# Optimization experiments

Hardware: AMD Instinct MI355X
Metric: run time of the kernel (lower is better)

Reference implementation:

```python
import jax, jax.numpy as jnp
import numpy as np

N_NODES = 100000
N_EDGES = 3200000
DIM = 64


def setup_inputs() -> dict:
    key = jax.random.key(0)
    k1, k2, k3, k4, k5, k6 = jax.random.split(key, 6)
    lap_rows = jax.random.randint(k1, (N_EDGES,), 0, N_NODES, dtype=jnp.int32)
    lap_cols = jax.random.randint(k2, (N_EDGES,), 0, N_NODES, dtype=jnp.int32)
    # normalized-Laplacian-like positive values
    lap_vals = jax.random.uniform(k3, (N_EDGES,), dtype=jnp.float32) * 0.1
    features = jax.random.normal(k4, (N_NODES, DIM), dtype=jnp.float32)
    scale = 1.0 / np.sqrt(DIM)
    W1 = jax.random.normal(k5, (DIM, DIM), dtype=jnp.float32) * scale
    b1 = jnp.zeros((DIM,), dtype=jnp.float32)
    W2 = jax.random.normal(k6, (DIM, DIM), dtype=jnp.float32) * scale
    b2 = jnp.zeros((DIM,), dtype=jnp.float32)
    return {
        "lap_rows": lap_rows, "lap_cols": lap_cols, "lap_vals": lap_vals,
        "features": features, "W1": W1, "b1": b1, "W2": W2, "b2": b2,
    }


def reference(lap_rows, lap_cols, lap_vals, features, W1, b1, W2, b2):
    # x = L @ features  (COO SpMM: gather source rows, scale, scatter-add to dest)
    msgs = lap_vals[:, None] * features[lap_cols]            # [E, D]
    x = jax.ops.segment_sum(msgs, lap_rows, num_segments=N_NODES)  # [N, D]
    # output = (L+I) E W1 + (L E * E) W2
    inter_part1 = (features + x) @ W1 + b1                   # [N, D_out]
    inter_part2 = (x * features) @ W2 + b2                   # [N, D_out]
    return inter_part1 + inter_part2
```

## Files before the change

kernel.cpp:

```cpp
#include <hip/hip_runtime.h>
#include <hip/hip_fp16.h>

#define DIM 64
#define RPB 64
#define RPB_SHIFT 6
#define SUP_SHIFT 11
#define SB_MAX 64
#define CAP 3072
#define CAPK (CAP / 1024)
#define HTILE_H 16384
#define HTILE1 8192
#define HTILE2 4096

typedef _Float16 half8 __attribute__((ext_vector_type(8)));
typedef float    f32x4 __attribute__((ext_vector_type(4)));
typedef float    f32x2 __attribute__((ext_vector_type(2)));

template <bool HI>
__device__ __forceinline__ __half2 q2h(unsigned int w)
{
    f32x2 f = __builtin_amdgcn_cvt_pk_f32_fp8(w, HI);
    return __floats2half2_rn(f[0], f[1]);
}

__global__ __launch_bounds__(256) void scatter_kernel(
    const int* __restrict__ rows, const int* __restrict__ cols,
    const float* __restrict__ vals, const float* __restrict__ feat,
    float* __restrict__ x, int E)
{
    unsigned long long t = (unsigned long long)blockIdx.x * blockDim.x + threadIdx.x;
    int e = (int)(t >> 6);
    int d = (int)(t & 63);
    if (e >= E) return;
    int r = rows[e];
    int c = cols[e];
    float v = vals[e];
    float f = feat[(size_t)c * DIM + d];
    atomicAdd(&x[(size_t)r * DIM + d], v * f);
}

__global__ __launch_bounds__(256) void cvt_kernel(
    const float* __restrict__ f, __half* __restrict__ h, int n2)
{
    int i = blockIdx.x * blockDim.x + threadIdx.x;
    if (i < n2) {
        float2 v = ((const float2*)f)[i];
        __half2 o;
        o.x = __float2half(v.x);
        o.y = __float2half(v.y);
        ((__half2*)h)[i] = o;
    }
}

__global__ __launch_bounds__(1024) void prep_kernel(
    const float* __restrict__ feat, __half* __restrict__ featH,
    unsigned char* __restrict__ featQ,
    const int* __restrict__ rows, int* __restrict__ gcnt,
    int n8, int NC, int E, int B)
{
    if ((int)blockIdx.x < NC) {
        int i = blockIdx.x * 1024 + threadIdx.x;
        if (i < n8) {
            const float4* src = (const float4*)(feat + (size_t)i * 8);
            float4 a = src[0], b = src[1];
            __half2 h0 = __floats2half2_rn(a.x, a.y);
            __half2 h1 = __floats2half2_rn(a.z, a.w);
            __half2 h2 = __floats2half2_rn(b.x, b.y);
            __half2 h3 = __floats2half2_rn(b.z, b.w);
            float4 ho;
            ho.x = __builtin_bit_cast(float, h0);
            ho.y = __builtin_bit_cast(float, h1);
            ho.z = __builtin_bit_cast(float, h2);
            ho.w = __builtin_bit_cast(float, h3);
            *(float4*)(featH + (size_t)i * 8) = ho;
            unsigned int q0 = __builtin_amdgcn_cvt_pk_fp8_f32(a.x, a.y, 0, false);
            q0 = __builtin_amdgcn_cvt_pk_fp8_f32(a.z, a.w, (int)q0, true);
            unsigned int q1 = __builtin_amdgcn_cvt_pk_fp8_f32(b.x, b.y, 0, false);
            q1 = __builtin_amdgcn_cvt_pk_fp8_f32(b.z, b.w, (int)q1, true);
            uint2 qo; qo.x = q0; qo.y = q1;
            *(uint2*)(featQ + (size_t)i * 8) = qo;
        }
    } else {
        extern __shared__ int lcnt[];
        for (int i = threadIdx.x; i < B; i += 1024) lcnt[i] = 0;
        __syncthreads();
        int base = ((int)blockIdx.x - NC) * HTILE_H;
#pragma unroll
        for (int k = 0; k < HTILE_H / 1024; ++k) {
            int e = base + k * 1024 + threadIdx.x;
            if (e < E) atomicAdd(&lcnt[rows[e] >> RPB_SHIFT], 1);
        }
        __syncthreads();
        for (int i = threadIdx.x; i < B; i += 1024)
            if (lcnt[i]) atomicAdd(&gcnt[i], lcnt[i]);
    }
}

__global__ __launch_bounds__(1024) void scan_kernel(
    const int* __restrict__ gcnt, int* __restrict__ offs, int* __restrict__ cursors,
    int* __restrict__ soffs, int* __restrict__ scursors, int B, int SB, int E)
{
    __shared__ int lds[2048];
    int t = threadIdx.x;
    int c0 = (t < B) ? gcnt[t] : 0;
    int c1 = (t + 1024 < B) ? gcnt[t + 1024] : 0;
    lds[t] = c0;
    lds[t + 1024] = c1;
    __syncthreads();
    for (int off = 1; off < 2048; off <<= 1) {
        int a = (t >= off) ? lds[t - off] : 0;
        int b = lds[t + 1024 - off];
        __syncthreads();
        lds[t] += a;
        lds[t + 1024] += b;
        __syncthreads();
    }
    if (t < B) {
        int e = lds[t] - c0;
        offs[t] = e; cursors[t] = e;
        if ((t & 31) == 0) { soffs[t >> 5] = e; scursors[t >> 5] = e; }
    }
    int t2 = t + 1024;
    if (t2 < B) {
        int e = lds[t2] - c1;
        offs[t2] = e; cursors[t2] = e;
        if ((t2 & 31) == 0) { soffs[t2 >> 5] = e; scursors[t2 >> 5] = e; }
    }
    if (t == 0) { offs[B] = E; soffs[SB] = E; }
}

__global__ __launch_bounds__(1024) void superbin_kernel(
    const int* __restrict__ rows, const int* __restrict__ cols,
    const float* __restrict__ vals, int* __restrict__ scursors,
    unsigned long long* __restrict__ sorted1, int E, int SB)
{
    __shared__ int cnt[SB_MAX];
    __shared__ int bse[SB_MAX];
    const int tid = threadIdx.x;
    if (tid < SB) cnt[tid] = 0;
    __syncthreads();
    const int tbase = blockIdx.x * HTILE1;
    int rr[HTILE1 / 1024];
#pragma unroll
    for (int k = 0; k < HTILE1 / 1024; ++k) {
        int e = tbase + k * 1024 + tid;
        rr[k] = (e < E) ? rows[e] : -1;
        if (rr[k] >= 0) atomicAdd(&cnt[rr[k] >> SUP_SHIFT], 1);
    }
    __syncthreads();
    if (tid < SB) {
        int c = cnt[tid];
        bse[tid] = c ? atomicAdd(&scursors[tid], c) : 0;
        cnt[tid] = 0;
    }
    __syncthreads();
#pragma unroll
    for (int k = 0; k < HTILE1 / 1024; ++k) {
        int e = tbase + k * 1024 + tid;
        if (rr[k] >= 0) {
            int r  = rr[k];
            int sb = r >> SUP_SHIFT;
            int slot = bse[sb] + atomicAdd(&cnt[sb], 1);
            unsigned long long pk =
                ((unsigned long long)__float_as_uint(vals[e]) << 32) |
                ((unsigned long long)(r & 2047) << 17) |
                (unsigned)cols[e];
            sorted1[slot] = pk;
        }
    }
}

__global__ __launch_bounds__(1024) void finebin_kernel(
    const unsigned long long* __restrict__ sorted1, const int* __restrict__ soffs,
    int* __restrict__ cursors, unsigned long long* __restrict__ sorted2,
    int E, int B, int SB)
{
    extern __shared__ int l[];
    int* cnt  = l;
    int* bse  = l + B;
    int* sofl = l + 2 * B;
    const int tid = threadIdx.x;
    if (tid <= SB) sofl[tid] = soffs[tid];
    for (int i = tid; i < B; i += 1024) cnt[i] = 0;
    __syncthreads();

    const int tbase = blockIdx.x * HTILE2;
    int sb0 = 0;
    {
        int lo = 0, hi = SB - 1;
        while (lo < hi) {
            int mid = (lo + hi + 1) >> 1;
            if (sofl[mid] <= tbase) lo = mid; else hi = mid - 1;
        }
        sb0 = lo;
    }

    unsigned long long pkr[HTILE2 / 1024];
    int fidr[HTILE2 / 1024];
#pragma unroll
    for (int k = 0; k < HTILE2 / 1024; ++k) {
        int i = tbase + k * 1024 + tid;
        if (i < E) {
            pkr[k] = sorted1[i];
            int sb = sb0;
            while (sofl[sb + 1] <= i) sb++;
            fidr[k] = (sb << 5) + (int)((pkr[k] >> 23) & 31);
            atomicAdd(&cnt[fidr[k]], 1);
        } else fidr[k] = -1;
    }
    __syncthreads();
    for (int i = tid; i < B; i += 1024) {
        int c = cnt[i];
        bse[i] = c ? atomicAdd(&cursors[i], c) : 0;
    }
    __syncthreads();
    for (int i = tid; i < B; i += 1024) cnt[i] = 0;
    __syncthreads();
#pragma unroll
    for (int k = 0; k < HTILE2 / 1024; ++k) {
        if (fidr[k] >= 0) {
            int f = fidr[k];
            int slot = bse[f] + atomicAdd(&cnt[f], 1);
            sorted2[slot] = pkr[k];
        }
    }
}

__global__ __launch_bounds__(1024, 8) void reduce_fused_mfma_kernel(
    const unsigned long long* __restrict__ sorted, const int* __restrict__ offs,
    const unsigned char* __restrict__ featQ, const __half* __restrict__ featH,
    const float* __restrict__ W1, const float* __restrict__ b1,
    const float* __restrict__ W2, const float* __restrict__ b2,
    float* __restrict__ out, int N)
{
    __shared__ unsigned long long spk[CAP];
    __shared__ int rcnt[RPB];
    __shared__ int rbase[RPB];
    __shared__ float xs[RPB][DIM + 4];
    __shared__ half8 Wl[1024];
    __shared__ float biasl[DIM];

    const int tid = threadIdx.x;
    const int b   = blockIdx.x;
    const int w    = tid >> 6;
    const int lane = tid & 63;

    {
        int t    = tid >> 8;
        int c    = (tid >> 6) & 3;
        int quad = (tid >> 4) & 3;
        int m    = tid & 15;
        const float* Wsrc = (t < 2) ? W1 : W2;
        int kbase = (t & 1) * 32 + quad * 8;
        int col   = c * 16 + m;
        half8 wv;
#pragma unroll
        for (int j = 0; j < 8; ++j)
            wv[j] = (_Float16)Wsrc[(kbase + j) * DIM + col];
        Wl[tid] = wv;
        if (tid < DIM) biasl[tid] = b1[tid] + b2[tid];
    }

    const int s    = offs[b];
    const int tend = offs[b + 1];
    int nl = tend - s;
    if (nl > CAP) nl = CAP;

    if (tid < RPB) rcnt[tid] = 0;
    __syncthreads();

    unsigned long long pkreg[CAPK];
#pragma unroll
    for (int k = 0; k < CAPK; ++k) {
        int i = k * 1024 + tid;
        pkreg[k] = (i < nl) ? sorted[s + i] : 0ull;
    }
#pragma unroll
    for (int k = 0; k < CAPK; ++k) {
        int i = k * 1024 + tid;
        if (i < nl) atomicAdd(&rcnt[(int)((pkreg[k] >> 17) & (RPB - 1))], 1);
    }
    __syncthreads();

    if (tid < 64) {
        int c = rcnt[tid];
        int v = c;
#pragma unroll
        for (int off = 1; off < 64; off <<= 1) {
            int u = __shfl_up(v, off, 64);
            if (tid >= off) v += u;
        }
        rbase[tid] = v - c;
        rcnt[tid]  = 0;
    }
    __syncthreads();

#pragma unroll
    for (int k = 0; k < CAPK; ++k) {
        int i = k * 1024 + tid;
        if (i < nl) {
            int rl  = (int)((pkreg[k] >> 17) & (RPB - 1));
            int idx = atomicAdd(&rcnt[rl], 1);
            spk[rbase[rl] + idx] = pkreg[k];
        }
    }
    __syncthreads();

    const int eg   = lane >> 3;
    const int sub  = lane & 7;
    const int rowbase = b * RPB;

#pragma unroll
    for (int j = 0; j < RPB / 16; ++j) {
        int rl = w + 16 * j;
        int rs = rbase[rl];
        int rt = rs + rcnt[rl];

        __half2 hacc[4];
#pragma unroll
        for (int q = 0; q < 4; ++q) hacc[q] = __floats2half2_rn(0.f, 0.f);

        int i = rs + eg;
        for (; i + 24 < rt; i += 32) {
            unsigned long long pk0 = spk[i];
            unsigned long long pk1 = spk[i + 8];
            unsigned long long pk2 = spk[i + 16];
            unsigned long long pk3 = spk[i + 24];
            uint2 q0 = *(const uint2*)(featQ + ((size_t)(pk0 & 0x1FFFFu) << 6) + sub * 8);
            uint2 q1 = *(const uint2*)(featQ + ((size_t)(pk1 & 0x1FFFFu) << 6) + sub * 8);
            uint2 q2 = *(const uint2*)(featQ + ((size_t)(pk2 & 0x1FFFFu) << 6) + sub * 8);
            uint2 q3 = *(const uint2*)(featQ + ((size_t)(pk3 & 0x1FFFFu) << 6) + sub * 8);
            __half2 v0 = __float2half2_rn(__uint_as_float((unsigned)(pk0 >> 32)));
            __half2 v1 = __float2half2_rn(__uint_as_float((unsigned)(pk1 >> 32)));
            __half2 v2 = __float2half2_rn(__uint_as_float((unsigned)(pk2 >> 32)));
            __half2 v3 = __float2half2_rn(__uint_as_float((unsigned)(pk3 >> 32)));
            hacc[0] = __hfma2(v0, q2h<false>(q0.x), hacc[0]);
            hacc[1] = __hfma2(v0, q2h<true >(q0.x), hacc[1]);
            hacc[2] = __hfma2(v0, q2h<false>(q0.y), hacc[2]);
            hacc[3] = __hfma2(v0, q2h<true >(q0.y), hacc[3]);
            hacc[0] = __hfma2(v1, q2h<false>(q1.x), hacc[0]);
            hacc[1] = __hfma2(v1, q2h<true >(q1.x), hacc[1]);
            hacc[2] = __hfma2(v1, q2h<false>(q1.y), hacc[2]);
            hacc[3] = __hfma2(v1, q2h<true >(q1.y), hacc[3]);
            hacc[0] = __hfma2(v2, q2h<false>(q2.x), hacc[0]);
            hacc[1] = __hfma2(v2, q2h<true >(q2.x), hacc[1]);
            hacc[2] = __hfma2(v2, q2h<false>(q2.y), hacc[2]);
            hacc[3] = __hfma2(v2, q2h<true >(q2.y), hacc[3]);
            hacc[0] = __hfma2(v3, q2h<false>(q3.x), hacc[0]);
            hacc[1] = __hfma2(v3, q2h<true >(q3.x), hacc[1]);
            hacc[2] = __hfma2(v3, q2h<false>(q3.y), hacc[2]);
            hacc[3] = __hfma2(v3, q2h<true >(q3.y), hacc[3]);
        }
        for (; i < rt; i += 8) {
            unsigned long long pk0 = spk[i];
            uint2 q0 = *(const uint2*)(featQ + ((size_t)(pk0 & 0x1FFFFu) << 6) + sub * 8);
            __half2 v0 = __float2half2_rn(__uint_as_float((unsigned)(pk0 >> 32)));
            hacc[0] = __hfma2(v0, q2h<false>(q0.x), hacc[0]);
            hacc[1] = __hfma2(v0, q2h<true >(q0.x), hacc[1]);
            hacc[2] = __hfma2(v0, q2h<false>(q0.y), hacc[2]);
            hacc[3] = __hfma2(v0, q2h<true >(q0.y), hacc[3]);
        }

        float acc[8];
#pragma unroll
        for (int q = 0; q < 4; ++q) {
            acc[2 * q]     = __low2float(hacc[q]);
            acc[2 * q + 1] = __high2float(hacc[q]);
        }
#pragma unroll
        for (int off = 8; off < 64; off <<= 1) {
#pragma unroll
            for (int q = 0; q < 8; ++q)
                acc[q] += __shfl_xor(acc[q], off, 64);
        }

        if (eg == 0) {
            float4 o; o.x = acc[0]; o.y = acc[1]; o.z = acc[2]; o.w = acc[3];
            *(float4*)&xs[rl][sub * 8] = o;
        } else if (eg == 1) {
            float4 o; o.x = acc[4]; o.y = acc[5]; o.z = acc[6]; o.w = acc[7];
            *(float4*)&xs[rl][sub * 8 + 4] = o;
        }
    }
    __syncthreads();

    if (tend - s > CAP) {
        for (int e = s + CAP + tid; e < tend; e += 1024) {
            unsigned long long pk = sorted[e];
            int rl = (int)((pk >> 17) & (RPB - 1));
            float v = __uint_as_float((unsigned)(pk >> 32));
            int c = (int)(pk & 0x1FFFFu);
            for (int d = 0; d < DIM; ++d)
                atomicAdd(&xs[rl][d], v * __half2float(featH[(size_t)c * DIM + d]));
        }
        __syncthreads();
    }

    {
        const int m    = lane & 15;
        const int quad = lane >> 4;
        const int tile = w >> 2;
        const int cw   = w & 3;

        const int fb = cw * 64 + quad * 16 + m;
        half8 wf0 = Wl[fb];
        half8 wf1 = Wl[fb + 256];
        half8 wf2 = Wl[fb + 512];
        half8 wf3 = Wl[fb + 768];
        float bias = biasl[cw * 16 + m];

        int rowl = tile * 16 + m;
        int grow = rowbase + rowl;
        int rldr = (grow < N) ? grow : (N - 1);
        const __half* fp = featH + (size_t)rldr * DIM + quad * 8;
        half8 flo = *(const half8*)(fp);
        half8 fhi = *(const half8*)(fp + 32);
        const float* xp = &xs[rowl][quad * 8];
        float4 xl0 = *(const float4*)(xp);
        float4 xl1 = *(const float4*)(xp + 4);
        float4 xh0 = *(const float4*)(xp + 32);
        float4 xh1 = *(const float4*)(xp + 36);

        half8 alo, ahi, blo, bhi;
        _Float16 xv;
        xv = (_Float16)xl0.x; alo[0] = flo[0] + xv; blo[0] = flo[0] * xv;
        xv = (_Float16)xl0.y; alo[1] = flo[1] + xv; blo[1] = flo[1] * xv;
        xv = (_Float16)xl0.z; alo[2] = flo[2] + xv; blo[2] = flo[2] * xv;
        xv = (_Float16)xl0.w; alo[3] = flo[3] + xv; blo[3] = flo[3] * xv;
        xv = (_Float16)xl1.x; alo[4] = flo[4] + xv; blo[4] = flo[4] * xv;
        xv = (_Float16)xl1.y; alo[5] = flo[5] + xv; blo[5] = flo[5] * xv;
        xv = (_Float16)xl1.z; alo[6] = flo[6] + xv; blo[6] = flo[6] * xv;
        xv = (_Float16)xl1.w; alo[7] = flo[7] + xv; blo[7] = flo[7] * xv;
        xv = (_Float16)xh0.x; ahi[0] = fhi[0] + xv; bhi[0] = fhi[0] * xv;
        xv = (_Float16)xh0.y; ahi[1] = fhi[1] + xv; bhi[1] = fhi[1] * xv;
        xv = (_Float16)xh0.z; ahi[2] = fhi[2] + xv; bhi[2] = fhi[2] * xv;
        xv = (_Float16)xh0.w; ahi[3] = fhi[3] + xv; bhi[3] = fhi[3] * xv;
        xv = (_Float16)xh1.x; ahi[4] = fhi[4] + xv; bhi[4] = fhi[4] * xv;
        xv = (_Float16)xh1.y; ahi[5] = fhi[5] + xv; bhi[5] = fhi[5] * xv;
        xv = (_Float16)xh1.z; ahi[6] = fhi[6] + xv; bhi[6] = fhi[6] * xv;
        xv = (_Float16)xh1.w; ahi[7] = fhi[7] + xv; bhi[7] = fhi[7] * xv;

        f32x4 a0 = { bias, bias, bias, bias };
        a0 = __builtin_amdgcn_mfma_f32_16x16x32_f16(alo, wf0, a0, 0, 0, 0);
        a0 = __builtin_amdgcn_mfma_f32_16x16x32_f16(ahi, wf1, a0, 0, 0, 0);
        a0 = __builtin_amdgcn_mfma_f32_16x16x32_f16(blo, wf2, a0, 0, 0, 0);
        a0 = __builtin_amdgcn_mfma_f32_16x16x32_f16(bhi, wf3, a0, 0, 0, 0);

#pragma unroll
        for (int reg = 0; reg < 4; ++reg) {
            int orow = rowbase + tile * 16 + quad * 4 + reg;
            if (orow < N)
                out[(size_t)orow * DIM + cw * 16 + m] = a0[reg];
        }
    }
}

__global__ __launch_bounds__(256) void transform_mfma_kernel(
    const __half* __restrict__ featH, const float* __restrict__ x,
    const float* __restrict__ W1, const float* __restrict__ b1,
    const float* __restrict__ W2, const float* __restrict__ b2,
    float* __restrict__ out, int N)
{
    const int lane = threadIdx.x & 63;
    const int m    = lane & 15;
    const int quad = lane >> 4;

    half8 wfrag[4][4];
#pragma unroll
    for (int t = 0; t < 4; ++t) {
        const float* Wsrc = (t < 2) ? W1 : W2;
        int kbase = (t & 1) * 32 + quad * 8;
#pragma unroll
        for (int c = 0; c < 4; ++c) {
            int col = c * 16 + m;
            half8 w;
#pragma unroll
            for (int j = 0; j < 8; ++j)
                w[j] = (_Float16)Wsrc[(kbase + j) * DIM + col];
            wfrag[t][c] = w;
        }
    }
    float bias[4];
#pragma unroll
    for (int c = 0; c < 4; ++c)
        bias[c] = b1[c * 16 + m] + b2[c * 16 + m];

    const int ntiles = (N + 15) / 16;
    const int wid    = (int)((blockIdx.x * blockDim.x + threadIdx.x) >> 6);
    const int nwaves = (int)((gridDim.x * blockDim.x) >> 6);

    for (int tile = wid; tile < ntiles; tile += nwaves) {
        int row  = tile * 16 + m;
        int rldr = (row < N) ? row : (N - 1);
        const __half* fp = featH + (size_t)rldr * DIM + quad * 8;
        const float*  xp = x     + (size_t)rldr * DIM + quad * 8;
        half8 flo = *(const half8*)(fp);
        half8 fhi = *(const half8*)(fp + 32);
        float4 xl0 = *(const float4*)(xp);
        float4 xl1 = *(const float4*)(xp + 4);
        float4 xh0 = *(const float4*)(xp + 32);
        float4 xh1 = *(const float4*)(xp + 36);

        half8 alo, ahi, blo, bhi;
        _Float16 xv;
        xv = (_Float16)xl0.x; alo[0] = flo[0] + xv; blo[0] = flo[0] * xv;
        xv = (_Float16)xl0.y; alo[1] = flo[1] + xv; blo[1] = flo[1] * xv;
        xv = (_Float16)xl0.z; alo[2] = flo[2] + xv; blo[2] = flo[2] * xv;
        xv = (_Float16)xl0.w; alo[3] = flo[3] + xv; blo[3] = flo[3] * xv;
        xv = (_Float16)xl1.x; alo[4] = flo[4] + xv; blo[4] = flo[4] * xv;
        xv = (_Float16)xl1.y; alo[5] = flo[5] + xv; blo[5] = flo[5] * xv;
        xv = (_Float16)xl1.z; alo[6] = flo[6] + xv; blo[6] = flo[6] * xv;
        xv = (_Float16)xl1.w; alo[7] = flo[7] + xv; blo[7] = flo[7] * xv;
        xv = (_Float16)xh0.x; ahi[0] = fhi[0] + xv; bhi[0] = fhi[0] * xv;
        xv = (_Float16)xh0.y; ahi[1] = fhi[1] + xv; bhi[1] = fhi[1] * xv;
        xv = (_Float16)xh0.z; ahi[2] = fhi[2] + xv; bhi[2] = fhi[2] * xv;
        xv = (_Float16)xh0.w; ahi[3] = fhi[3] + xv; bhi[3] = fhi[3] * xv;
        xv = (_Float16)xh1.x; ahi[4] = fhi[4] + xv; bhi[4] = fhi[4] * xv;
        xv = (_Float16)xh1.y; ahi[5] = fhi[5] + xv; bhi[5] = fhi[5] * xv;
        xv = (_Float16)xh1.z; ahi[6] = fhi[6] + xv; bhi[6] = fhi[6] * xv;
        xv = (_Float16)xh1.w; ahi[7] = fhi[7] + xv; bhi[7] = fhi[7] * xv;

        f32x4 acc[4];
#pragma unroll
        for (int c = 0; c < 4; ++c) {
            f32x4 a0 = { bias[c], bias[c], bias[c], bias[c] };
            a0 = __builtin_amdgcn_mfma_f32_16x16x32_f16(alo, wfrag[0][c], a0, 0, 0, 0);
            a0 = __builtin_amdgcn_mfma_f32_16x16x32_f16(ahi, wfrag[1][c], a0, 0, 0, 0);
            a0 = __builtin_amdgcn_mfma_f32_16x16x32_f16(blo, wfrag[2][c], a0, 0, 0, 0);
            a0 = __builtin_amdgcn_mfma_f32_16x16x32_f16(bhi, wfrag[3][c], a0, 0, 0, 0);
            acc[c] = a0;
        }

#pragma unroll
        for (int reg = 0; reg < 4; ++reg) {
            int orow = tile * 16 + quad * 4 + reg;
            if (orow < N) {
#pragma unroll
                for (int c = 0; c < 4; ++c)
                    out[(size_t)orow * DIM + c * 16 + m] = acc[c][reg];
            }
        }
    }
}

extern "C" void kernel_launch(void* const* d_in, const int* in_sizes, int n_in,
                              void* d_out, int out_size, void* d_ws, size_t ws_size,
                              hipStream_t stream)
{
    const int*   rows = (const int*)d_in[0];
    const int*   cols = (const int*)d_in[1];
    const float* vals = (const float*)d_in[2];
    const float* feat = (const float*)d_in[3];
    const float* W1   = (const float*)d_in[4];
    const float* b1   = (const float*)d_in[5];
    const float* W2   = (const float*)d_in[6];
    const float* b2   = (const float*)d_in[7];
    float* out = (float*)d_out;

    const int E  = in_sizes[0];
    const int N  = in_sizes[3] / DIM;
    const int B  = (N + RPB - 1) / RPB;
    const int SB = (B + 31) / 32;

    char* ws = (char*)d_ws;
    size_t xBytes     = (size_t)N * DIM * sizeof(float);
    size_t hBytes     = (((size_t)N * DIM * sizeof(__half)) + 255) / 256 * 256;
    size_t qBytes     = (((size_t)N * DIM) + 255) / 256 * 256;
    size_t offsBytes  = (((size_t)(B + 1) * sizeof(int)) + 255) / 256 * 256;
    size_t cursBytes  = (((size_t)B * sizeof(int)) + 255) / 256 * 256;
    size_t soffBytes  = (((size_t)(SB + 1) * sizeof(int)) + 255) / 256 * 256;
    size_t scurBytes  = (((size_t)SB * sizeof(int)) + 255) / 256 * 256;
    size_t sortBytes  = (size_t)E * 8;

    float*              x        = (float*)ws;
    __half*             featH    = (__half*)(ws + xBytes);
    unsigned char*      featQ    = (unsigned char*)(ws + xBytes + hBytes);
    int*                offs     = (int*)(ws + xBytes + hBytes + qBytes);
    int*                cursors  = (int*)(ws + xBytes + hBytes + qBytes + offsBytes);
    int*                soffs    = (int*)(ws + xBytes + hBytes + qBytes + offsBytes + cursBytes);
    int*                scursors = (int*)(ws + xBytes + hBytes + qBytes + offsBytes + cursBytes + soffBytes);
    unsigned long long* sorted1  = (unsigned long long*)(ws + xBytes + hBytes + qBytes + offsBytes +
                                                         cursBytes + soffBytes + scurBytes);
    unsigned long long* sorted2  = sorted1 + E;
    size_t need = xBytes + hBytes + qBytes + offsBytes + cursBytes + soffBytes + scurBytes + 2 * sortBytes;

    if (ws_size >= need && B <= 2048 && SB <= SB_MAX && N <= 131072) {
        const int n8  = N * DIM / 8;
        const int NC  = (n8 + 1023) / 1024;
        const int NTH = (E + HTILE_H - 1) / HTILE_H;
        const int NT1 = (E + HTILE1 - 1) / HTILE1;
        const int NT2 = (E + HTILE2 - 1) / HTILE2;
        hipMemsetAsync(offs, 0, (size_t)(B + 1) * sizeof(int), stream);
        prep_kernel<<<NC + NTH, 1024, (size_t)B * 4, stream>>>(
            feat, featH, featQ, rows, offs, n8, NC, E, B);
        scan_kernel<<<1, 1024, 0, stream>>>(offs, offs, cursors, soffs, scursors, B, SB, E);
        superbin_kernel<<<NT1, 1024, 0, stream>>>(rows, cols, vals, scursors, sorted1, E, SB);
        finebin_kernel<<<NT2, 1024, (size_t)(2 * B + SB + 1) * 4, stream>>>(
            sorted1, soffs, cursors, sorted2, E, B, SB);
        reduce_fused_mfma_kernel<<<B, 1024, 0, stream>>>(sorted2, offs, featQ, featH,
                                                         W1, b1, W2, b2, out, N);
    } else {
        cvt_kernel<<<(N * DIM / 2 + 255) / 256, 256, 0, stream>>>(feat, featH, N * DIM / 2);
        hipMemsetAsync(x, 0, xBytes, stream);
        unsigned long long threads = (unsigned long long)E * DIM;
        unsigned int blocks = (unsigned int)((threads + 255ull) / 256ull);
        scatter_kernel<<<blocks, 256, 0, stream>>>(rows, cols, vals, feat, x, E);
        transform_mfma_kernel<<<640, 256, 0, stream>>>(featH, x, W1, b1, W2, b2, out, N);
    }
}
```

Before: 241.7 us.

## Process four rows per wave concurrently in SpMM gather, plus nontemporal edge loads

Restructures the per-row gather so that each wave handles four rows at once: two 8-lane groups per row, uniform trip count by wave-wide max, predicated loads unrolled by 2. The cross-lane reduction shrinks from three shuffle stages to one, and the serial loop over four row passes goes away. It also marks the edge-list load as nontemporal. The cost is load imbalance, since every group iterates to the longest row in the wave, and the unroll depth per group is lower.

```diff
diff --git a/kernel.cpp b/kernel.cpp
--- a/kernel.cpp
+++ b/kernel.cpp
@@ -273,7 +273,7 @@
 #pragma unroll
     for (int k = 0; k < CAPK; ++k) {
         int i = k * 1024 + tid;
-        pkreg[k] = (i < nl) ? sorted[s + i] : 0ull;
+        pkreg[k] = (i < nl) ? __builtin_nontemporal_load(sorted + s + i) : 0ull;
     }
 #pragma unroll
     for (int k = 0; k < CAPK; ++k) {
@@ -310,30 +310,37 @@
     const int sub  = lane & 7;
     const int rowbase = b * RPB;
 
-#pragma unroll
-    for (int j = 0; j < RPB / 16; ++j) {
-        int rl = w + 16 * j;
-        int rs = rbase[rl];
-        int rt = rs + rcnt[rl];
+#define GATHER(PK) (*(const uint2*)(featQ + ((size_t)((PK) & 0x1FFFFu) << 6) + sub * 8))
+
+    {
+        const int rl = 4 * w + (eg >> 1);
+        const int g  = eg & 1;
+        const int rs = rbase[rl];
+        const int rt = rs + rcnt[rl];
+
+        int cg = rt - (rs + g);
+        cg = (cg > 0) ? ((cg + 1) >> 1) : 0;
+        int kmax = (cg + 1) >> 1;
+#pragma unroll
+        for (int off = 1; off < 64; off <<= 1) {
+            int u = __shfl_xor(kmax, off, 64);
+            kmax = (u > kmax) ? u : kmax;
+        }
 
         __half2 hacc[4];
 #pragma unroll
         for (int q = 0; q < 4; ++q) hacc[q] = __floats2half2_rn(0.f, 0.f);
 
-        int i = rs + eg;
-        for (; i + 24 < rt; i += 32) {
-            unsigned long long pk0 = spk[i];
-            unsigned long long pk1 = spk[i + 8];
-            unsigned long long pk2 = spk[i + 16];
-            unsigned long long pk3 = spk[i + 24];
-            uint2 q0 = *(const uint2*)(featQ + ((size_t)(pk0 & 0x1FFFFu) << 6) + sub * 8);
-            uint2 q1 = *(const uint2*)(featQ + ((size_t)(pk1 & 0x1FFFFu) << 6) + sub * 8);
-            uint2 q2 = *(const uint2*)(featQ + ((size_t)(pk2 & 0x1FFFFu) << 6) + sub * 8);
-            uint2 q3 = *(const uint2*)(featQ + ((size_t)(pk3 & 0x1FFFFu) << 6) + sub * 8);
+        int idx = rs + g;
+        for (int k = 0; k < kmax; ++k, idx += 4) {
+            bool p0 = idx < rt;
+            bool p1 = idx + 2 < rt;
+            unsigned long long pk0 = p0 ? spk[idx] : 0ull;
+            unsigned long long pk1 = p1 ? spk[idx + 2] : 0ull;
+            uint2 q0 = GATHER(pk0);
+            uint2 q1 = GATHER(pk1);
             __half2 v0 = __float2half2_rn(__uint_as_float((unsigned)(pk0 >> 32)));
             __half2 v1 = __float2half2_rn(__uint_as_float((unsigned)(pk1 >> 32)));
-            __half2 v2 = __float2half2_rn(__uint_as_float((unsigned)(pk2 >> 32)));
-            __half2 v3 = __float2half2_rn(__uint_as_float((unsigned)(pk3 >> 32)));
             hacc[0] = __hfma2(v0, q2h<false>(q0.x), hacc[0]);
             hacc[1] = __hfma2(v0, q2h<true >(q0.x), hacc[1]);
             hacc[2] = __hfma2(v0, q2h<false>(q0.y), hacc[2]);
@@ -342,23 +349,6 @@
             hacc[1] = __hfma2(v1, q2h<true >(q1.x), hacc[1]);
             hacc[2] = __hfma2(v1, q2h<false>(q1.y), hacc[2]);
             hacc[3] = __hfma2(v1, q2h<true >(q1.y), hacc[3]);
-            hacc[0] = __hfma2(v2, q2h<false>(q2.x), hacc[0]);
-            hacc[1] = __hfma2(v2, q2h<true >(q2.x), hacc[1]);
-            hacc[2] = __hfma2(v2, q2h<false>(q2.y), hacc[2]);
-            hacc[3] = __hfma2(v2, q2h<true >(q2.y), hacc[3]);
-            hacc[0] = __hfma2(v3, q2h<false>(q3.x), hacc[0]);
-            hacc[1] = __hfma2(v3, q2h<true >(q3.x), hacc[1]);
-            hacc[2] = __hfma2(v3, q2h<false>(q3.y), hacc[2]);
-            hacc[3] = __hfma2(v3, q2h<true >(q3.y), hacc[3]);
-        }
-        for (; i < rt; i += 8) {
-            unsigned long long pk0 = spk[i];
-            uint2 q0 = *(const uint2*)(featQ + ((size_t)(pk0 & 0x1FFFFu) << 6) + sub * 8);
-            __half2 v0 = __float2half2_rn(__uint_as_float((unsigned)(pk0 >> 32)));
-            hacc[0] = __hfma2(v0, q2h<false>(q0.x), hacc[0]);
-            hacc[1] = __hfma2(v0, q2h<true >(q0.x), hacc[1]);
-            hacc[2] = __hfma2(v0, q2h<false>(q0.y), hacc[2]);
-            hacc[3] = __hfma2(v0, q2h<true >(q0.y), hacc[3]);
         }
 
         float acc[8];
@@ -368,20 +358,17 @@
             acc[2 * q + 1] = __high2float(hacc[q]);
         }
 #pragma unroll
-        for (int off = 8; off < 64; off <<= 1) {
-#pragma unroll
-            for (int q = 0; q < 8; ++q)
-                acc[q] += __shfl_xor(acc[q], off, 64);
-        }
-
-        if (eg == 0) {
-            float4 o; o.x = acc[0]; o.y = acc[1]; o.z = acc[2]; o.w = acc[3];
-            *(float4*)&xs[rl][sub * 8] = o;
-        } else if (eg == 1) {
-            float4 o; o.x = acc[4]; o.y = acc[5]; o.z = acc[6]; o.w = acc[7];
-            *(float4*)&xs[rl][sub * 8 + 4] = o;
-        }
-    }
+        for (int q = 0; q < 8; ++q)
+            acc[q] += __shfl_xor(acc[q], 8, 64);
+
+        if (g == 0) {
+            float4 o0; o0.x = acc[0]; o0.y = acc[1]; o0.z = acc[2]; o0.w = acc[3];
+            float4 o1; o1.x = acc[4]; o1.y = acc[5]; o1.z = acc[6]; o1.w = acc[7];
+            *(float4*)&xs[rl][sub * 8]     = o0;
+            *(float4*)&xs[rl][sub * 8 + 4] = o1;
+        }
+    }
+#undef GATHER
     __syncthreads();
 
     if (tend - s > CAP) {
```

Result: faster. 228.3 us (-5.5%).
